# Kernel tuning notes

Hardware: AMD Instinct MI355X
Metric: run time of the kernel (lower is better)

## Reference

```python
import jax, jax.numpy as jnp
import numpy as np

N = 2              # tree branching factor per axis
DEPTH = 2          # fixed tree depth (uniform octree -> 4^3 leaf grid)
DATA_DIM = 28      # 3 * basis_dim + 1 (SH9 rgb + sigma)
BASIS_DIM = 9
MAX_STEPS = 16     # >= max DDA crossings of the 4^3 leaf grid
STEP_SIZE = 0.001
BG = 1.0           # background_brightness
B = 262144

SH_C0 = 0.28209479177387814
SH_C1 = 0.4886025119029199
SH_C2 = (1.0925484305920792, -1.0925484305920792, 0.31539156525252005,
         -1.0925484305920792, 0.5462742152960396)


def eval_sh9(d):
    # d: [B,3] unit view directions -> [B,9] real SH basis (svox ordering)
    x, y, z = d[..., 0], d[..., 1], d[..., 2]
    return jnp.stack([
        jnp.full_like(x, SH_C0),
        -SH_C1 * y, SH_C1 * z, -SH_C1 * x,
        SH_C2[0] * x * y, SH_C2[1] * y * z,
        SH_C2[2] * (2.0 * z * z - x * x - y * y),
        SH_C2[3] * x * z, SH_C2[4] * (x * x - y * y),
    ], axis=-1)


def dda_unit(cen, invdir):
    # ray/unit-cube intersection; cen,invdir: [B,3] -> (tmin[B]>=0, tmax[B])
    t1 = -cen * invdir
    t2 = t1 + invdir
    tmin = jnp.maximum(jnp.max(jnp.minimum(t1, t2), axis=-1), 0.0)
    tmax = jnp.minimum(jnp.min(jnp.maximum(t1, t2), axis=-1), 1e9)
    return tmin, tmax


def tree_query(pos, data, child):
    # pos: [B,3] in [0,1); returns leaf values [B,DATA_DIM], corner [B,3], length [B]
    nb = pos.shape[0]
    node = jnp.zeros((nb,), jnp.int32)
    cur = pos
    corner = jnp.zeros_like(pos)
    length = jnp.ones((nb,), pos.dtype)
    done = jnp.zeros((nb,), bool)
    val = jnp.zeros((nb, DATA_DIM), pos.dtype)
    for _ in range(DEPTH):
        idx = jnp.clip(jnp.floor(cur * N).astype(jnp.int32), 0, N - 1)
        ch = child[node, idx[:, 0], idx[:, 1], idx[:, 2]]
        v = data[node, idx[:, 0], idx[:, 1], idx[:, 2]]
        new_len = length / N
        new_corner = corner + idx.astype(pos.dtype) * new_len[:, None]
        upd = ~done
        val = jnp.where(upd[:, None], v, val)
        corner = jnp.where(upd[:, None], new_corner, corner)
        length = jnp.where(upd, new_len, length)
        cur = jnp.where(upd[:, None], cur * N - idx.astype(pos.dtype), cur)
        node = jnp.where(upd, node + ch, node)
        done = done | (ch == 0)
    return val, corner, length


def setup_inputs() -> dict:
    key = jax.random.key(0)
    k0, k1, k2 = jax.random.split(key, 3)
    origins = (jax.random.uniform(k0, (B, 3), jnp.float32) - 0.5) * 0.6
    dirs = jax.random.normal(k1, (B, 3), jnp.float32)
    viewdirs = dirs / jnp.linalg.norm(dirs, axis=-1, keepdims=True)
    n_nodes = 1 + N ** 3
    data = jax.random.normal(k2, (n_nodes, N, N, N, DATA_DIM), jnp.float32) * 0.5
    child = np.zeros((n_nodes, N, N, N), np.int32)
    child[0] = np.arange(1, 1 + N ** 3, dtype=np.int32).reshape(N, N, N)  # relative offsets
    return {
        'origins': origins, 'dirs': dirs, 'viewdirs': viewdirs,
        'data': data, 'child': jnp.asarray(child),
        'offset': jnp.full((3,), 0.5, jnp.float32),
        'invradius': jnp.float32(0.5),
    }


def reference(origins, dirs, viewdirs, data, child, offset, invradius):
    origins_t = offset + origins * invradius          # world2tree
    dirs_n = dirs / jnp.linalg.norm(dirs, axis=-1, keepdims=True)
    invdirs = 1.0 / (dirs_n + 1e-9)
    t, tmax = dda_unit(origins_t, invdirs)
    sh_mult = eval_sh9(viewdirs)                      # [B,9]
    delta_scale = 1.0 / invradius
    light = jnp.ones((origins.shape[0],), origins.dtype)
    out = jnp.zeros((origins.shape[0], 3), origins.dtype)

    def step(carry, _):
        t, light, out = carry
        active = t < tmax
        pos = origins_t + t[:, None] * dirs_n
        pos_c = jnp.clip(pos, 0.0, 1.0 - 1e-6)
        val, corner, length = tree_query(pos_c, data, child)
        pos_local = (pos - corner) / length[:, None]
        smin, smax = dda_unit(pos_local, invdirs)
        delta_t = (smax - smin) * length + STEP_SIZE
        sigma = jax.nn.relu(val[:, -1])
        att = jnp.exp(-delta_t * sigma * delta_scale)
        weight = light * (1.0 - att)
        rgb_sh = val[:, :-1].reshape(-1, 3, BASIS_DIM)
        rgb = jax.nn.sigmoid(jnp.sum(sh_mult[:, None, :] * rgb_sh, axis=-1))
        w = jnp.where(active, weight, 0.0)
        out = out + w[:, None] * rgb
        light = jnp.where(active, light * att, light)
        t = jnp.where(active, t + delta_t, t)
        return (t, light, out), None

    (t, light, out), _ = jax.lax.scan(step, (t, light, out), None, length=MAX_STEPS)
    return out + light[:, None] * BG
```

## Files before the change

### kernel.cpp

```cpp
#include <hip/hip_runtime.h>
#include <math.h>

typedef _Float16 f16;
typedef _Float16 f16x2 __attribute__((ext_vector_type(2)));

constexpr int   DATA_DIM  = 28;
constexpr int   MAX_STEPS = 16;
constexpr float STEP_SIZE = 0.001f;
constexpr float BG        = 1.0f;
constexpr int   CELLS     = 8;
constexpr int   NVOX      = 64;
constexpr int   VOX_H     = 28;

__device__ __forceinline__ float fdot2(unsigned w, f16x2 s, float acc) {
#if __has_builtin(__builtin_amdgcn_fdot2)
    return __builtin_amdgcn_fdot2(__builtin_bit_cast(f16x2, w), s, acc, false);
#else
    f16x2 a = __builtin_bit_cast(f16x2, w);
    return acc + (float)a.x * (float)s.x + (float)a.y * (float)s.y;
#endif
}

__global__ __launch_bounds__(256) void vr_kernel(
    const float* __restrict__ origins,
    const float* __restrict__ dirs,
    const float* __restrict__ viewdirs,
    const float* __restrict__ data,
    const int*   __restrict__ child,
    const float* __restrict__ offset,
    const float* __restrict__ invradius_p,
    float* __restrict__ out,
    int B)
{
    __shared__ f16   s_vh[NVOX * VOX_H];
    __shared__ float s_len[NVOX];
    __shared__ int   s_fent[NVOX];

    const int t0 = threadIdx.x;
    if (t0 < NVOX) {
        int vx = t0 >> 4, vy = (t0 >> 2) & 3, vz = t0 & 3;
        int e  = ((vx >> 1) * 2 + (vy >> 1)) * 2 + (vz >> 1);
        int ch = child[e];
        int   fe  = e;
        float len = 0.5f;
        if (ch != 0) {
            int node = ch;
            e  = node * CELLS + ((vx & 1) * 2 + (vy & 1)) * 2 + (vz & 1);
            fe  = e;
            len = 0.25f;
        }
        s_fent[t0] = fe;
        s_len[t0]  = len;
    }
    __syncthreads();
    for (int i = t0; i < NVOX * VOX_H; i += 256) {
        int v = i / VOX_H;
        int j = i - v * VOX_H;
        s_vh[i] = (f16)data[s_fent[v] * DATA_DIM + j];
    }
    __syncthreads();

    int tid = blockIdx.x * 256 + t0;
    if (tid >= B) return;

    float ox = origins[tid*3+0], oy = origins[tid*3+1], oz = origins[tid*3+2];
    float dx = dirs[tid*3+0],    dy = dirs[tid*3+1],    dz = dirs[tid*3+2];
    float vdx = viewdirs[tid*3+0], vdy = viewdirs[tid*3+1], vdz = viewdirs[tid*3+2];
    float invr = invradius_p[0];
    float otx = offset[0] + ox * invr;
    float oty = offset[1] + oy * invr;
    float otz = offset[2] + oz * invr;

    float sh[9];
    {
        const float C0 = 0.28209479177387814f;
        const float C1 = 0.4886025119029199f;
        sh[0] = C0;
        sh[1] = -C1 * vdy;
        sh[2] =  C1 * vdz;
        sh[3] = -C1 * vdx;
        sh[4] =  1.0925484305920792f * vdx * vdy;
        sh[5] = -1.0925484305920792f * vdy * vdz;
        sh[6] =  0.31539156525252005f * (2.0f*vdz*vdz - vdx*vdx - vdy*vdy);
        sh[7] = -1.0925484305920792f * vdx * vdz;
        sh[8] =  0.5462742152960396f * (vdx*vdx - vdy*vdy);
    }
    f16x2 shA[5], shB[5];
    shA[0] = f16x2{(f16)sh[0], (f16)sh[1]};
    shA[1] = f16x2{(f16)sh[2], (f16)sh[3]};
    shA[2] = f16x2{(f16)sh[4], (f16)sh[5]};
    shA[3] = f16x2{(f16)sh[6], (f16)sh[7]};
    shA[4] = f16x2{(f16)sh[8], (f16)0.0f};
    shB[0] = f16x2{(f16)0.0f,  (f16)sh[0]};
    shB[1] = f16x2{(f16)sh[1], (f16)sh[2]};
    shB[2] = f16x2{(f16)sh[3], (f16)sh[4]};
    shB[3] = f16x2{(f16)sh[5], (f16)sh[6]};
    shB[4] = f16x2{(f16)sh[7], (f16)sh[8]};

    float nrm = sqrtf(dx*dx + dy*dy + dz*dz);
    float dnx = dx / nrm, dny = dy / nrm, dnz = dz / nrm;
    float ivx = 1.0f / (dnx + 1e-9f);
    float ivy = 1.0f / (dny + 1e-9f);
    float ivz = 1.0f / (dnz + 1e-9f);

    float t, tmax;
    {
        float t1x = -otx * ivx, t2x = t1x + ivx;
        float t1y = -oty * ivy, t2y = t1y + ivy;
        float t1z = -otz * ivz, t2z = t1z + ivz;
        float mn = fmaxf(fmaxf(fminf(t1x,t2x), fminf(t1y,t2y)), fminf(t1z,t2z));
        float mx = fminf(fminf(fmaxf(t1x,t2x), fmaxf(t1y,t2y)), fmaxf(t1z,t2z));
        t    = fmaxf(mn, 0.0f);
        tmax = fminf(mx, 1000000000.0f);
    }

    const float katt = -(1.0f / invr);
    float light = 1.0f;
    float o0 = 0.0f, o1 = 0.0f, o2 = 0.0f;

    #pragma unroll 1
    for (int s = 0; s < MAX_STEPS; ++s) {
        if (!(t < tmax)) break;

        float px = fmaf(t, dnx, otx);
        float py = fmaf(t, dny, oty);
        float pz = fmaf(t, dnz, otz);
        float pcx = fminf(fmaxf(px, 0.0f), 0.999999f);
        float pcy = fminf(fmaxf(py, 0.0f), 0.999999f);
        float pcz = fminf(fmaxf(pz, 0.0f), 0.999999f);

        int vx = (int)(pcx * 4.0f);
        int vy = (int)(pcy * 4.0f);
        int vz = (int)(pcz * 4.0f);
        int lidx = (vx << 4) + (vy << 2) + vz;

        float len    = s_len[lidx];
        float invlen = __builtin_amdgcn_rcpf(len);

        float cfx = floorf(pcx * invlen);
        float cfy = floorf(pcy * invlen);
        float cfz = floorf(pcz * invlen);
        float plx = fmaf(px, invlen, -cfx);
        float ply = fmaf(py, invlen, -cfy);
        float plz = fmaf(pz, invlen, -cfz);

        float t1x = -plx * ivx, t2x = t1x + ivx;
        float t1y = -ply * ivy, t2y = t1y + ivy;
        float t1z = -plz * ivz, t2z = t1z + ivz;
        float mn = fmaxf(fmaxf(fminf(t1x,t2x), fminf(t1y,t2y)), fminf(t1z,t2z));
        float mx = fminf(fminf(fmaxf(t1x,t2x), fmaxf(t1y,t2y)), fmaxf(t1z,t2z));
        float smin = fmaxf(mn, 0.0f);
        float smax = fminf(mx, 1000000000.0f);
        float dt = fmaf(smax - smin, len, STEP_SIZE);

        const uint2* rec = (const uint2*)(s_vh + lidx * VOX_H);
        uint2 q0 = rec[0], q1 = rec[1], q2 = rec[2], q3 = rec[3];
        uint2 q4 = rec[4], q5 = rec[5], q6 = rec[6];
        unsigned D0=q0.x, D1=q0.y, D2=q1.x, D3=q1.y, D4=q2.x, D5=q2.y, D6=q3.x;
        unsigned D7=q3.y, D8=q4.x, D9=q4.y, D10=q5.x, D11=q5.y, D12=q6.x, D13=q6.y;

        float a0 = 0.0f, a1 = 0.0f, a2 = 0.0f;
        a0 = fdot2(D0, shA[0], a0); a0 = fdot2(D1, shA[1], a0);
        a0 = fdot2(D2, shA[2], a0); a0 = fdot2(D3, shA[3], a0);
        a0 = fdot2(D4, shA[4], a0);
        a1 = fdot2(D4, shB[0], a1); a1 = fdot2(D5, shB[1], a1);
        a1 = fdot2(D6, shB[2], a1); a1 = fdot2(D7, shB[3], a1);
        a1 = fdot2(D8, shB[4], a1);
        a2 = fdot2(D9, shA[0], a2); a2 = fdot2(D10, shA[1], a2);
        a2 = fdot2(D11, shA[2], a2); a2 = fdot2(D12, shA[3], a2);
        a2 = fdot2(D13, shA[4], a2);

        f16x2 last = __builtin_bit_cast(f16x2, D13);
        float sigma = fmaxf((float)last.y, 0.0f);

        float att    = __expf(katt * dt * sigma);
        float weight = light * (1.0f - att);

        float r0 = __builtin_amdgcn_rcpf(1.0f + __expf(-a0));
        float r1 = __builtin_amdgcn_rcpf(1.0f + __expf(-a1));
        float r2 = __builtin_amdgcn_rcpf(1.0f + __expf(-a2));

        o0 = fmaf(weight, r0, o0);
        o1 = fmaf(weight, r1, o1);
        o2 = fmaf(weight, r2, o2);
        light *= att;
        t += dt;
    }

    out[tid*3+0] = fmaf(light, BG, o0);
    out[tid*3+1] = fmaf(light, BG, o1);
    out[tid*3+2] = fmaf(light, BG, o2);
}

extern "C" void kernel_launch(void* const* d_in, const int* in_sizes, int n_in,
                              void* d_out, int out_size, void* d_ws, size_t ws_size,
                              hipStream_t stream) {
    const float* origins  = (const float*)d_in[0];
    const float* dirs     = (const float*)d_in[1];
    const float* viewdirs = (const float*)d_in[2];
    const float* data     = (const float*)d_in[3];
    const int*   child    = (const int*)d_in[4];
    const float* offset   = (const float*)d_in[5];
    const float* invrad   = (const float*)d_in[6];
    float* out = (float*)d_out;
    int B = in_sizes[0] / 3;
    int block = 256;
    int grid = (B + block - 1) / block;
    vr_kernel<<<grid, block, 0, stream>>>(origins, dirs, viewdirs, data, child,
                                          offset, invrad, out, B);
}
```

Before: 13.62 us.

## Software-pipeline ray march with LDS prefetch and bitmask-derived cell size

Restructures the march loop into a fully unrolled, double-buffered pipeline: the next step's geometry and shared-memory voxel fetch are issued before the current step's shading math, hiding LDS latency. Per-voxel cell length is now derived from a wave-wide ballot bitmask in registers instead of an LDS lookup, and floor/rcp are replaced by shifts and constants. The per-lane break becomes a wave-uniform any() exit with predication, so inactive lanes do redundant work, and register pressure rises from the two record buffers.

```diff
diff --git a/kernel.cpp b/kernel.cpp
--- a/kernel.cpp
+++ b/kernel.cpp
@@ -20,6 +20,78 @@
     return acc + (float)a.x * (float)s.x + (float)a.y * (float)s.y;
 #endif
 }
+
+#define GEOM(TC, LIDX, DTV)                                                  \
+  {                                                                          \
+    float px = fmaf((TC), dnx, otx);                                         \
+    float py = fmaf((TC), dny, oty);                                         \
+    float pz = fmaf((TC), dnz, otz);                                         \
+    float pcx = fminf(fmaxf(px, 0.0f), 0.999999f);                           \
+    float pcy = fminf(fmaxf(py, 0.0f), 0.999999f);                           \
+    float pcz = fminf(fmaxf(pz, 0.0f), 0.999999f);                           \
+    int vx = (int)(pcx * 4.0f);                                              \
+    int vy = (int)(pcy * 4.0f);                                              \
+    int vz = (int)(pcz * 4.0f);                                              \
+    (LIDX) = (vx << 4) | (vy << 2) | vz;                                     \
+    bool d2 = (d2mask >> (LIDX)) & 1ull;                                     \
+    float invlen = d2 ? 4.0f : 2.0f;                                         \
+    float lenv   = d2 ? 0.25f : 0.5f;                                        \
+    int   shf    = d2 ? 0 : 1;                                               \
+    float cfx = (float)(vx >> shf);                                          \
+    float cfy = (float)(vy >> shf);                                          \
+    float cfz = (float)(vz >> shf);                                          \
+    float plx = fmaf(px, invlen, -cfx);                                      \
+    float ply = fmaf(py, invlen, -cfy);                                      \
+    float plz = fmaf(pz, invlen, -cfz);                                      \
+    float t1x = -plx * ivx, t2x = t1x + ivx;                                 \
+    float t1y = -ply * ivy, t2y = t1y + ivy;                                 \
+    float t1z = -plz * ivz, t2z = t1z + ivz;                                 \
+    float mn = fmaxf(fmaxf(fminf(t1x,t2x), fminf(t1y,t2y)), fminf(t1z,t2z)); \
+    float mx = fminf(fminf(fmaxf(t1x,t2x), fmaxf(t1y,t2y)), fmaxf(t1z,t2z)); \
+    float smin = fmaxf(mn, 0.0f);                                            \
+    float smax = fminf(mx, 1000000000.0f);                                   \
+    (DTV) = fmaf(smax - smin, lenv, STEP_SIZE);                              \
+  }
+
+#define PREF(LI, Q0,Q1,Q2,Q3,Q4,Q5,Q6)                                       \
+  {                                                                          \
+    const uint2* _r = (const uint2*)(s_vh + (LI) * VOX_H);                   \
+    Q0=_r[0]; Q1=_r[1]; Q2=_r[2]; Q3=_r[3]; Q4=_r[4]; Q5=_r[5]; Q6=_r[6];   \
+  }
+
+#define STEP(QA0,QA1,QA2,QA3,QA4,QA5,QA6, QB0,QB1,QB2,QB3,QB4,QB5,QB6)      \
+  {                                                                          \
+    bool act = t_cur < tmax;                                                 \
+    if (!__any(act)) break;                                                  \
+    float t_next = act ? t_cur + dtc : t_cur;                                \
+    int lin; float dtn;                                                      \
+    GEOM(t_next, lin, dtn);                                                  \
+    PREF(lin, QB0,QB1,QB2,QB3,QB4,QB5,QB6);                                  \
+    unsigned D0=QA0.x, D1=QA0.y, D2=QA1.x, D3=QA1.y, D4=QA2.x, D5=QA2.y,     \
+             D6=QA3.x, D7=QA3.y, D8=QA4.x, D9=QA4.y, D10=QA5.x, D11=QA5.y,   \
+             D12=QA6.x, D13=QA6.y;                                           \
+    float a0=0.f, a1=0.f, a2=0.f;                                            \
+    a0=fdot2(D0,shA0,a0); a0=fdot2(D1,shA1,a0); a0=fdot2(D2,shA2,a0);        \
+    a0=fdot2(D3,shA3,a0); a0=fdot2(D4,shA4,a0);                              \
+    a1=fdot2(D4,shB0,a1); a1=fdot2(D5,shB1,a1); a1=fdot2(D6,shB2,a1);        \
+    a1=fdot2(D7,shB3,a1); a1=fdot2(D8,shB4,a1);                              \
+    a2=fdot2(D9,shA0,a2); a2=fdot2(D10,shA1,a2); a2=fdot2(D11,shA2,a2);      \
+    a2=fdot2(D12,shA3,a2); a2=fdot2(D13,shA4,a2);                            \
+    f16x2 lastp = __builtin_bit_cast(f16x2, D13);                            \
+    float sigma = fmaxf((float)lastp.y, 0.0f);                               \
+    float att = __expf(katt * dtc * sigma);                                  \
+    float weight = light * (1.0f - att);                                     \
+    float w = act ? weight : 0.0f;                                           \
+    float r0 = __builtin_amdgcn_rcpf(1.0f + __expf(-a0));                    \
+    float r1 = __builtin_amdgcn_rcpf(1.0f + __expf(-a1));                    \
+    float r2 = __builtin_amdgcn_rcpf(1.0f + __expf(-a2));                    \
+    o0 = fmaf(w, r0, o0);                                                    \
+    o1 = fmaf(w, r1, o1);                                                    \
+    o2 = fmaf(w, r2, o2);                                                    \
+    light = act ? light * att : light;                                       \
+    t_cur = t_next;                                                          \
+    dtc = dtn;                                                               \
+  }
 
 __global__ __launch_bounds__(256) void vr_kernel(
     const float* __restrict__ origins,
@@ -32,30 +104,31 @@
     float* __restrict__ out,
     int B)
 {
-    __shared__ f16   s_vh[NVOX * VOX_H];
-    __shared__ float s_len[NVOX];
-    __shared__ int   s_fent[NVOX];
-
-    const int t0 = threadIdx.x;
+    __shared__ f16 s_vh[NVOX * VOX_H];
+    __shared__ int s_fent[NVOX];
+
+    const int t0   = threadIdx.x;
+    const int lane = t0 & 63;
+
+    unsigned long long d2mask;
+    {
+        int vx = lane >> 4, vy = (lane >> 2) & 3, vz = lane & 3;
+        int e0 = ((vx >> 1) << 2) | ((vy >> 1) << 1) | (vz >> 1);
+        int ch = child[e0];
+        d2mask = __ballot(ch != 0);
+    }
+
     if (t0 < NVOX) {
         int vx = t0 >> 4, vy = (t0 >> 2) & 3, vz = t0 & 3;
-        int e  = ((vx >> 1) * 2 + (vy >> 1)) * 2 + (vz >> 1);
-        int ch = child[e];
-        int   fe  = e;
-        float len = 0.5f;
-        if (ch != 0) {
-            int node = ch;
-            e  = node * CELLS + ((vx & 1) * 2 + (vy & 1)) * 2 + (vz & 1);
-            fe  = e;
-            len = 0.25f;
-        }
+        int e0 = ((vx >> 1) << 2) | ((vy >> 1) << 1) | (vz >> 1);
+        int ch = child[e0];
+        int fe = (ch != 0) ? ch * CELLS + (((vx & 1) << 2) | ((vy & 1) << 1) | (vz & 1))
+                           : e0;
         s_fent[t0] = fe;
-        s_len[t0]  = len;
     }
     __syncthreads();
     for (int i = t0; i < NVOX * VOX_H; i += 256) {
-        int v = i / VOX_H;
-        int j = i - v * VOX_H;
+        int v = i / VOX_H, j = i - v * VOX_H;
         s_vh[i] = (f16)data[s_fent[v] * DATA_DIM + j];
     }
     __syncthreads();
@@ -85,17 +158,16 @@
         sh[7] = -1.0925484305920792f * vdx * vdz;
         sh[8] =  0.5462742152960396f * (vdx*vdx - vdy*vdy);
     }
-    f16x2 shA[5], shB[5];
-    shA[0] = f16x2{(f16)sh[0], (f16)sh[1]};
-    shA[1] = f16x2{(f16)sh[2], (f16)sh[3]};
-    shA[2] = f16x2{(f16)sh[4], (f16)sh[5]};
-    shA[3] = f16x2{(f16)sh[6], (f16)sh[7]};
-    shA[4] = f16x2{(f16)sh[8], (f16)0.0f};
-    shB[0] = f16x2{(f16)0.0f,  (f16)sh[0]};
-    shB[1] = f16x2{(f16)sh[1], (f16)sh[2]};
-    shB[2] = f16x2{(f16)sh[3], (f16)sh[4]};
-    shB[3] = f16x2{(f16)sh[5], (f16)sh[6]};
-    shB[4] = f16x2{(f16)sh[7], (f16)sh[8]};
+    f16x2 shA0 = f16x2{(f16)sh[0], (f16)sh[1]};
+    f16x2 shA1 = f16x2{(f16)sh[2], (f16)sh[3]};
+    f16x2 shA2 = f16x2{(f16)sh[4], (f16)sh[5]};
+    f16x2 shA3 = f16x2{(f16)sh[6], (f16)sh[7]};
+    f16x2 shA4 = f16x2{(f16)sh[8], (f16)0.0f};
+    f16x2 shB0 = f16x2{(f16)0.0f,  (f16)sh[0]};
+    f16x2 shB1 = f16x2{(f16)sh[1], (f16)sh[2]};
+    f16x2 shB2 = f16x2{(f16)sh[3], (f16)sh[4]};
+    f16x2 shB3 = f16x2{(f16)sh[5], (f16)sh[6]};
+    f16x2 shB4 = f16x2{(f16)sh[7], (f16)sh[8]};
 
     float nrm = sqrtf(dx*dx + dy*dy + dz*dz);
     float dnx = dx / nrm, dny = dy / nrm, dnz = dz / nrm;
@@ -103,88 +175,30 @@
     float ivy = 1.0f / (dny + 1e-9f);
     float ivz = 1.0f / (dnz + 1e-9f);
 
-    float t, tmax;
+    float t_cur, tmax;
     {
         float t1x = -otx * ivx, t2x = t1x + ivx;
         float t1y = -oty * ivy, t2y = t1y + ivy;
         float t1z = -otz * ivz, t2z = t1z + ivz;
         float mn = fmaxf(fmaxf(fminf(t1x,t2x), fminf(t1y,t2y)), fminf(t1z,t2z));
         float mx = fminf(fminf(fmaxf(t1x,t2x), fmaxf(t1y,t2y)), fmaxf(t1z,t2z));
-        t    = fmaxf(mn, 0.0f);
-        tmax = fminf(mx, 1000000000.0f);
+        t_cur = fmaxf(mn, 0.0f);
+        tmax  = fminf(mx, 1000000000.0f);
     }
 
     const float katt = -(1.0f / invr);
     float light = 1.0f;
     float o0 = 0.0f, o1 = 0.0f, o2 = 0.0f;
 
-    #pragma unroll 1
-    for (int s = 0; s < MAX_STEPS; ++s) {
-        if (!(t < tmax)) break;
-
-        float px = fmaf(t, dnx, otx);
-        float py = fmaf(t, dny, oty);
-        float pz = fmaf(t, dnz, otz);
-        float pcx = fminf(fmaxf(px, 0.0f), 0.999999f);
-        float pcy = fminf(fmaxf(py, 0.0f), 0.999999f);
-        float pcz = fminf(fmaxf(pz, 0.0f), 0.999999f);
-
-        int vx = (int)(pcx * 4.0f);
-        int vy = (int)(pcy * 4.0f);
-        int vz = (int)(pcz * 4.0f);
-        int lidx = (vx << 4) + (vy << 2) + vz;
-
-        float len    = s_len[lidx];
-        float invlen = __builtin_amdgcn_rcpf(len);
-
-        float cfx = floorf(pcx * invlen);
-        float cfy = floorf(pcy * invlen);
-        float cfz = floorf(pcz * invlen);
-        float plx = fmaf(px, invlen, -cfx);
-        float ply = fmaf(py, invlen, -cfy);
-        float plz = fmaf(pz, invlen, -cfz);
-
-        float t1x = -plx * ivx, t2x = t1x + ivx;
-        float t1y = -ply * ivy, t2y = t1y + ivy;
-        float t1z = -plz * ivz, t2z = t1z + ivz;
-        float mn = fmaxf(fmaxf(fminf(t1x,t2x), fminf(t1y,t2y)), fminf(t1z,t2z));
-        float mx = fminf(fminf(fmaxf(t1x,t2x), fmaxf(t1y,t2y)), fmaxf(t1z,t2z));
-        float smin = fmaxf(mn, 0.0f);
-        float smax = fminf(mx, 1000000000.0f);
-        float dt = fmaf(smax - smin, len, STEP_SIZE);
-
-        const uint2* rec = (const uint2*)(s_vh + lidx * VOX_H);
-        uint2 q0 = rec[0], q1 = rec[1], q2 = rec[2], q3 = rec[3];
-        uint2 q4 = rec[4], q5 = rec[5], q6 = rec[6];
-        unsigned D0=q0.x, D1=q0.y, D2=q1.x, D3=q1.y, D4=q2.x, D5=q2.y, D6=q3.x;
-        unsigned D7=q3.y, D8=q4.x, D9=q4.y, D10=q5.x, D11=q5.y, D12=q6.x, D13=q6.y;
-
-        float a0 = 0.0f, a1 = 0.0f, a2 = 0.0f;
-        a0 = fdot2(D0, shA[0], a0); a0 = fdot2(D1, shA[1], a0);
-        a0 = fdot2(D2, shA[2], a0); a0 = fdot2(D3, shA[3], a0);
-        a0 = fdot2(D4, shA[4], a0);
-        a1 = fdot2(D4, shB[0], a1); a1 = fdot2(D5, shB[1], a1);
-        a1 = fdot2(D6, shB[2], a1); a1 = fdot2(D7, shB[3], a1);
-        a1 = fdot2(D8, shB[4], a1);
-        a2 = fdot2(D9, shA[0], a2); a2 = fdot2(D10, shA[1], a2);
-        a2 = fdot2(D11, shA[2], a2); a2 = fdot2(D12, shA[3], a2);
-        a2 = fdot2(D13, shA[4], a2);
-
-        f16x2 last = __builtin_bit_cast(f16x2, D13);
-        float sigma = fmaxf((float)last.y, 0.0f);
-
-        float att    = __expf(katt * dt * sigma);
-        float weight = light * (1.0f - att);
-
-        float r0 = __builtin_amdgcn_rcpf(1.0f + __expf(-a0));
-        float r1 = __builtin_amdgcn_rcpf(1.0f + __expf(-a1));
-        float r2 = __builtin_amdgcn_rcpf(1.0f + __expf(-a2));
-
-        o0 = fmaf(weight, r0, o0);
-        o1 = fmaf(weight, r1, o1);
-        o2 = fmaf(weight, r2, o2);
-        light *= att;
-        t += dt;
+    uint2 A0,A1,A2,A3,A4,A5,A6, B0,B1,B2,B3,B4,B5,B6;
+    int li0; float dtc;
+    GEOM(t_cur, li0, dtc);
+    PREF(li0, A0,A1,A2,A3,A4,A5,A6);
+
+    #pragma unroll
+    for (int s = 0; s < MAX_STEPS; s += 2) {
+        STEP(A0,A1,A2,A3,A4,A5,A6, B0,B1,B2,B3,B4,B5,B6);
+        STEP(B0,B1,B2,B3,B4,B5,B6, A0,A1,A2,A3,A4,A5,A6);
     }
 
     out[tid*3+0] = fmaf(light, BG, o0);
```

Result: slower. 13.98 us (+2.7%).
